# Kernel tuning notes

Hardware: AMD Instinct MI355X
Metric: run time of the kernel (lower is better)

Reference implementation:

```python
import jax, jax.numpy as jnp
import numpy as np
from jax import lax

KERNEL = 3
K = 3


def setup_inputs() -> dict:
    key = jax.random.key(0)
    xcorr = jax.random.normal(key, (16, 1, 256, 8192), dtype=jnp.float32)
    return {"xcorr": xcorr}


def reference(xcorr):
    # xcorr: [B, C, H, W] (W = lag axis)
    W = xcorr.shape[-1]
    nlag = W // 2
    # max_pool2d with kernel (1,KERNEL), stride 1, padding (0, KERNEL//2).
    # torch pads with -inf for max pooling.
    neg_inf = jnp.asarray(-jnp.inf, dtype=xcorr.dtype)
    pad = KERNEL // 2
    smax = lax.reduce_window(
        xcorr,
        neg_inf,
        lax.max,
        window_dimensions=(1, 1, 1, KERNEL),
        window_strides=(1, 1, 1, 1),
        padding=[(0, 0), (0, 0), (0, 0), (pad, pad)],
    )
    keep = (smax == xcorr).astype(xcorr.dtype)  # local-max NMS mask
    scores = xcorr * keep
    topk_scores, topk_inds = lax.top_k(scores, K)  # sorted descending, [B,C,H,K]
    top = topk_inds[..., 0]  # best peak index [B,C,H]
    nearby = jnp.clip(
        jnp.stack([top - 1, top, top + 1], axis=-1), 0, W - 1
    )  # [B,C,H,3]
    neighbor_score = jnp.take_along_axis(xcorr, nearby, axis=-1)
    topk_index = topk_inds - nlag
    return neighbor_score, topk_scores, topk_index
```

## Files before the change

### kernel.cpp

```cpp
#include <hip/hip_runtime.h>
#include <climits>
#include <cmath>


#define PW    8192
#define PNLAG (PW / 2)
#define BLOCK 256
#define QPT   (PW / 4 / BLOCK)

__device__ __forceinline__ bool better(float av, int ai, float bv, int bi) {
  return (av > bv) || ((av == bv) && (ai < bi));
}

__device__ __forceinline__ void insert3_full(float v, int i,
                                             float &v0, int &i0,
                                             float &v1, int &i1,
                                             float &v2, int &i2) {
  if (better(v, i, v2, i2)) {
    if (better(v, i, v1, i1)) {
      if (better(v, i, v0, i0)) {
        v2 = v1; i2 = i1; v1 = v0; i1 = i0; v0 = v; i0 = i;
      } else {
        v2 = v1; i2 = i1; v1 = v; i1 = i;
      }
    } else {
      v2 = v; i2 = i;
    }
  }
}

__device__ __forceinline__ void insert3_fast(float c, int ci,
                                             float &v0, int &i0,
                                             float &v1, int &i1,
                                             float &v2, int &i2) {
  const bool b2 = c > v2;
  const bool b1 = c > v1;
  const bool b0 = c > v0;
  v2 = b1 ? v1 : (b2 ? c : v2);  i2 = b1 ? i1 : (b2 ? ci : i2);
  v1 = b0 ? v0 : (b1 ? c : v1);  i1 = b0 ? i0 : (b1 ? ci : i1);
  v0 = b0 ? c  : v0;             i0 = b0 ? ci : i0;
}

__global__ __launch_bounds__(BLOCK)
void detect_peaks_kernel(const float* __restrict__ x,
                         float* __restrict__ out,
                         int rows) {
  __shared__ float rv[12];
  __shared__ int   ri[12];

  const int row = blockIdx.x;
  const int t   = threadIdx.x;
  const float* __restrict__ xr = x + (size_t)row * PW;
  const float4* __restrict__ xv = (const float4*)xr;

  float v0 = -INFINITY, v1 = -INFINITY, v2 = -INFINITY;
  int   i0 = INT_MAX,   i1 = INT_MAX,   i2 = INT_MAX;

#pragma unroll
  for (int j = 0; j < QPT; ++j) {
    const int q = j * BLOCK + t;
    const int p = q * 4;
    const float4 v = xv[q];
    const float left  = (p > 0)        ? xr[p - 1] : -INFINITY;
    const float right = (p + 4 < PW)   ? xr[p + 4] : -INFINITY;

    const float p01 = fmaxf(v.x, v.y);
    const float p12 = fmaxf(v.y, v.z);
    const float p23 = fmaxf(v.z, v.w);
    const float m0 = fmaxf(left, p01);
    const float m1 = fmaxf(p01, v.z);
    const float m2 = fmaxf(p12, v.w);
    const float m3 = fmaxf(p23, right);

    const float s0 = (v.x == m0) ? v.x : 0.0f;
    const float s1 = (v.y == m1) ? v.y : 0.0f;
    const float s2 = (v.z == m2) ? v.z : 0.0f;
    const float s3 = (v.w == m3) ? v.w : 0.0f;

    const bool  a01 = s0 >= s1;
    const float hiA = a01 ? s0 : s1;   const int hiAi = a01 ? p     : p + 1;
    const float loA = a01 ? s1 : s0;   const int loAi = a01 ? p + 1 : p;
    const bool  a23 = s2 >= s3;
    const float hiB = a23 ? s2 : s3;   const int hiBi = a23 ? p + 2 : p + 3;
    const float loB = a23 ? s3 : s2;   const int loBi = a23 ? p + 3 : p + 2;

    const bool  ab  = hiA >= hiB;
    const float c1  = ab ? hiA : hiB;  const int c1i = ab ? hiAi : hiBi;
    const bool  sb  = ab ? (loA >= hiB) : (hiA >= loB);
    const float c2  = ab ? (sb ? loA : hiB) : (sb ? hiA : loB);
    const int   c2i = ab ? (sb ? loAi : hiBi) : (sb ? hiAi : loBi);

    insert3_fast(c1, c1i, v0, i0, v1, i1, v2, i2);
    insert3_fast(c2, c2i, v0, i0, v1, i1, v2, i2);
  }

  const int lane = t & 63;
  const int wave = t >> 6;
#pragma unroll
  for (int off = 32; off > 0; off >>= 1) {
    float ov0 = __shfl_down(v0, off);
    int   oi0 = __shfl_down(i0, off);
    float ov1 = __shfl_down(v1, off);
    int   oi1 = __shfl_down(i1, off);
    float ov2 = __shfl_down(v2, off);
    int   oi2 = __shfl_down(i2, off);
    if (lane + off < 64) {
      insert3_full(ov0, oi0, v0, i0, v1, i1, v2, i2);
      insert3_full(ov1, oi1, v0, i0, v1, i1, v2, i2);
      insert3_full(ov2, oi2, v0, i0, v1, i1, v2, i2);
    }
  }

  if (lane == 0) {
    rv[wave * 3 + 0] = v0; ri[wave * 3 + 0] = i0;
    rv[wave * 3 + 1] = v1; ri[wave * 3 + 1] = i1;
    rv[wave * 3 + 2] = v2; ri[wave * 3 + 2] = i2;
  }
  __syncthreads();

  if (t == 0) {
#pragma unroll
    for (int w = 1; w < 4; ++w) {
      insert3_full(rv[w * 3 + 0], ri[w * 3 + 0], v0, i0, v1, i1, v2, i2);
      insert3_full(rv[w * 3 + 1], ri[w * 3 + 1], v0, i0, v1, i1, v2, i2);
      insert3_full(rv[w * 3 + 2], ri[w * 3 + 2], v0, i0, v1, i1, v2, i2);
    }

    float* __restrict__ nb = out;
    float* __restrict__ ts = out + (size_t)rows * 3;
    float* __restrict__ ti = out + (size_t)rows * 6;

    const int top = i0;
#pragma unroll
    for (int k = 0; k < 3; ++k) {
      int idx = top - 1 + k;
      idx = idx < 0 ? 0 : (idx > PW - 1 ? PW - 1 : idx);
      nb[row * 3 + k] = xr[idx];
    }
    ts[row * 3 + 0] = v0;
    ts[row * 3 + 1] = v1;
    ts[row * 3 + 2] = v2;
    ti[row * 3 + 0] = (float)(i0 - PNLAG);
    ti[row * 3 + 1] = (float)(i1 - PNLAG);
    ti[row * 3 + 2] = (float)(i2 - PNLAG);
  }
}

extern "C" void kernel_launch(void* const* d_in, const int* in_sizes, int n_in,
                              void* d_out, int out_size, void* d_ws, size_t ws_size,
                              hipStream_t stream) {
  const float* x = (const float*)d_in[0];
  float* out = (float*)d_out;
  const int rows = in_sizes[0] / PW;
  detect_peaks_kernel<<<rows, BLOCK, 0, stream>>>(x, out, rows);
}
```

Measured before the change: 247.4 us.

## Load wave-contiguous float4 chunks up front and get neighbors via lane shuffles

Each wave now owns a contiguous 512-float4 segment and issues all eight vector loads before computing. The per-element left/right neighbor values are obtained by cross-lane shuffles instead of separate scalar global loads, with only the wave-boundary elements loaded from memory. This removes redundant scalar loads and increases memory-level parallelism, at the cost of extra shuffle instructions and more registers held live.

```diff
diff --git a/kernel.cpp b/kernel.cpp
--- a/kernel.cpp
+++ b/kernel.cpp
@@ -6,7 +6,8 @@
 #define PW    8192
 #define PNLAG (PW / 2)
 #define BLOCK 256
-#define QPT   (PW / 4 / BLOCK)
+#define NW    4
+#define J     8
 
 __device__ __forceinline__ bool better(float av, int ai, float bv, int bi) {
   return (av > bv) || ((av == bv) && (ai < bi));
@@ -48,21 +49,39 @@
   __shared__ float rv[12];
   __shared__ int   ri[12];
 
-  const int row = blockIdx.x;
-  const int t   = threadIdx.x;
+  const int row  = blockIdx.x;
+  const int t    = threadIdx.x;
+  const int lane = t & 63;
+  const int wave = t >> 6;
   const float* __restrict__ xr = x + (size_t)row * PW;
   const float4* __restrict__ xv = (const float4*)xr;
+
+  const int waveQ = wave * (J * 64);
+
+  float4 q[J];
+#pragma unroll
+  for (int j = 0; j < J; ++j) {
+    q[j] = xv[waveQ + j * 64 + lane];
+  }
+  float leftEdge  = -INFINITY;
+  float rightEdge = -INFINITY;
+  if (lane == 0 && wave > 0)      leftEdge  = xr[waveQ * 4 - 1];
+  if (lane == 63 && wave < NW - 1) rightEdge = xr[(waveQ + J * 64) * 4];
 
   float v0 = -INFINITY, v1 = -INFINITY, v2 = -INFINITY;
   int   i0 = INT_MAX,   i1 = INT_MAX,   i2 = INT_MAX;
 
 #pragma unroll
-  for (int j = 0; j < QPT; ++j) {
-    const int q = j * BLOCK + t;
-    const int p = q * 4;
-    const float4 v = xv[q];
-    const float left  = (p > 0)        ? xr[p - 1] : -INFINITY;
-    const float right = (p + 4 < PW)   ? xr[p + 4] : -INFINITY;
+  for (int j = 0; j < J; ++j) {
+    const int p = (waveQ + j * 64 + lane) * 4;
+    const float4 v = q[j];
+
+    const float lu = __shfl_up(v.w, 1);
+    const float l0 = (j > 0) ? __shfl(q[j - 1].w, 63) : leftEdge;
+    const float left = (lane == 0) ? l0 : lu;
+    const float rd = __shfl_down(v.x, 1);
+    const float r0 = (j < J - 1) ? __shfl(q[j + 1].x, 0) : rightEdge;
+    const float right = (lane == 63) ? r0 : rd;
 
     const float p01 = fmaxf(v.x, v.y);
     const float p12 = fmaxf(v.y, v.z);
@@ -94,8 +113,6 @@
     insert3_fast(c2, c2i, v0, i0, v1, i1, v2, i2);
   }
 
-  const int lane = t & 63;
-  const int wave = t >> 6;
 #pragma unroll
   for (int off = 32; off > 0; off >>= 1) {
     float ov0 = __shfl_down(v0, off);
@@ -120,7 +137,7 @@
 
   if (t == 0) {
 #pragma unroll
-    for (int w = 1; w < 4; ++w) {
+    for (int w = 1; w < NW; ++w) {
       insert3_full(rv[w * 3 + 0], ri[w * 3 + 0], v0, i0, v1, i1, v2, i2);
       insert3_full(rv[w * 3 + 1], ri[w * 3 + 1], v0, i0, v1, i1, v2, i2);
       insert3_full(rv[w * 3 + 2], ri[w * 3 + 2], v0, i0, v1, i1, v2, i2);
```

New measurement: 239.8 us. 1.03x faster.

## Use persistent 1024-thread blocks with next-row prefetch and shuffle-based halos

Applied to the files above, without the earlier changes.

The kernel changes from one 256-thread block per row to a persistent grid of 512 blocks with 1024 threads each that loop over rows. Each block loads the next row's data while it processes the current one. Neighbour halo values now come from wave shuffles instead of redundant global loads, and the final reduction across waves runs in parallel in wave 0 rather than serially in thread 0. The aim is to hide memory latency and cut extra loads, at the cost of double-buffered shared memory, one barrier per row, and fewer distinct blocks in flight.

```diff
diff --git a/kernel.cpp b/kernel.cpp
--- a/kernel.cpp
+++ b/kernel.cpp
@@ -3,10 +3,11 @@
 #include <cmath>
 
 
-#define PW    8192
-#define PNLAG (PW / 2)
-#define BLOCK 256
-#define QPT   (PW / 4 / BLOCK)
+#define PW     8192
+#define PNLAG  (PW / 2)
+#define TPB    1024
+#define NWAVES 16
+#define GRID   512
 
 __device__ __forceinline__ bool better(float av, int ai, float bv, int bi) {
   return (av > bv) || ((av == bv) && (ai < bi));
@@ -41,108 +42,152 @@
   v0 = b0 ? c  : v0;             i0 = b0 ? ci : i0;
 }
 
-__global__ __launch_bounds__(BLOCK)
+__device__ __forceinline__ void quad_cands(const float4 v, float left, float right, int p,
+                                           float &v0, int &i0, float &v1, int &i1,
+                                           float &v2, int &i2) {
+  const float p01 = fmaxf(v.x, v.y);
+  const float p12 = fmaxf(v.y, v.z);
+  const float p23 = fmaxf(v.z, v.w);
+  const float m0 = fmaxf(left, p01);
+  const float m1 = fmaxf(p01, v.z);
+  const float m2 = fmaxf(p12, v.w);
+  const float m3 = fmaxf(p23, right);
+  const float s0 = (v.x == m0) ? v.x : 0.0f;
+  const float s1 = (v.y == m1) ? v.y : 0.0f;
+  const float s2 = (v.z == m2) ? v.z : 0.0f;
+  const float s3 = (v.w == m3) ? v.w : 0.0f;
+  const bool  a01 = s0 >= s1;
+  const float hiA = a01 ? s0 : s1;   const int hiAi = a01 ? p     : p + 1;
+  const float loA = a01 ? s1 : s0;   const int loAi = a01 ? p + 1 : p;
+  const bool  a23 = s2 >= s3;
+  const float hiB = a23 ? s2 : s3;   const int hiBi = a23 ? p + 2 : p + 3;
+  const float loB = a23 ? s3 : s2;   const int loBi = a23 ? p + 3 : p + 2;
+  const bool  ab  = hiA >= hiB;
+  const float c1  = ab ? hiA : hiB;  const int c1i = ab ? hiAi : hiBi;
+  const bool  sb  = ab ? (loA >= hiB) : (hiA >= loB);
+  const float c2  = ab ? (sb ? loA : hiB) : (sb ? hiA : loB);
+  const int   c2i = ab ? (sb ? loAi : hiBi) : (sb ? hiAi : loBi);
+  insert3_fast(c1, c1i, v0, i0, v1, i1, v2, i2);
+  insert3_fast(c2, c2i, v0, i0, v1, i1, v2, i2);
+}
+
+__global__ __launch_bounds__(TPB)
 void detect_peaks_kernel(const float* __restrict__ x,
                          float* __restrict__ out,
                          int rows) {
-  __shared__ float rv[12];
-  __shared__ int   ri[12];
-
-  const int row = blockIdx.x;
-  const int t   = threadIdx.x;
-  const float* __restrict__ xr = x + (size_t)row * PW;
-  const float4* __restrict__ xv = (const float4*)xr;
-
-  float v0 = -INFINITY, v1 = -INFINITY, v2 = -INFINITY;
-  int   i0 = INT_MAX,   i1 = INT_MAX,   i2 = INT_MAX;
+  __shared__ float sv[2][NWAVES][3];
+  __shared__ int   si[2][NWAVES][3];
+
+  const int t     = threadIdx.x;
+  const int lane  = t & 63;
+  const int wave  = t >> 6;
+  const int qAidx = wave * 128 + lane;
+  const int qBidx = qAidx + 64;
+  const int spanL = wave * 512;
+
+  float* __restrict__ nb = out;
+  float* __restrict__ ts = out + (size_t)rows * 3;
+  float* __restrict__ ti = out + (size_t)rows * 6;
+
+  int row = blockIdx.x;
+
+  const float* xr0 = x + (size_t)row * PW;
+  float4 qA = ((const float4*)xr0)[qAidx];
+  float4 qB = ((const float4*)xr0)[qBidx];
+  float  eL = (lane == 0  && wave > 0)          ? xr0[spanL - 1]   : -INFINITY;
+  float  eR = (lane == 63 && wave < NWAVES - 1) ? xr0[spanL + 512] : -INFINITY;
+
+  int pb = 0;
+  while (row < rows) {
+    const float* __restrict__ xr_cur = x + (size_t)row * PW;
+    const int nrow = row + GRID;
+
+    float4 qA2 = {0, 0, 0, 0}, qB2 = {0, 0, 0, 0};
+    float  eL2 = -INFINITY, eR2 = -INFINITY;
+    if (nrow < rows) {
+      const float* __restrict__ xn = x + (size_t)nrow * PW;
+      qA2 = ((const float4*)xn)[qAidx];
+      qB2 = ((const float4*)xn)[qBidx];
+      if (lane == 0  && wave > 0)          eL2 = xn[spanL - 1];
+      if (lane == 63 && wave < NWAVES - 1) eR2 = xn[spanL + 512];
+    }
+
+    const float luA = __shfl_up(qA.w, 1);
+    const float rdA = __shfl_down(qA.x, 1);
+    const float bxB = __shfl(qB.x, 0);
+    const float luB = __shfl_up(qB.w, 1);
+    const float rdB = __shfl_down(qB.x, 1);
+    const float awB = __shfl(qA.w, 63);
+
+    const float lA = (lane == 0)  ? eL  : luA;
+    const float rA = (lane == 63) ? bxB : rdA;
+    const float lB = (lane == 0)  ? awB : luB;
+    const float rB = (lane == 63) ? eR  : rdB;
+
+    float v0 = -INFINITY, v1 = -INFINITY, v2 = -INFINITY;
+    int   i0 = INT_MAX,   i1 = INT_MAX,   i2 = INT_MAX;
+    quad_cands(qA, lA, rA, qAidx * 4, v0, i0, v1, i1, v2, i2);
+    quad_cands(qB, lB, rB, qBidx * 4, v0, i0, v1, i1, v2, i2);
 
 #pragma unroll
-  for (int j = 0; j < QPT; ++j) {
-    const int q = j * BLOCK + t;
-    const int p = q * 4;
-    const float4 v = xv[q];
-    const float left  = (p > 0)        ? xr[p - 1] : -INFINITY;
-    const float right = (p + 4 < PW)   ? xr[p + 4] : -INFINITY;
-
-    const float p01 = fmaxf(v.x, v.y);
-    const float p12 = fmaxf(v.y, v.z);
-    const float p23 = fmaxf(v.z, v.w);
-    const float m0 = fmaxf(left, p01);
-    const float m1 = fmaxf(p01, v.z);
-    const float m2 = fmaxf(p12, v.w);
-    const float m3 = fmaxf(p23, right);
-
-    const float s0 = (v.x == m0) ? v.x : 0.0f;
-    const float s1 = (v.y == m1) ? v.y : 0.0f;
-    const float s2 = (v.z == m2) ? v.z : 0.0f;
-    const float s3 = (v.w == m3) ? v.w : 0.0f;
-
-    const bool  a01 = s0 >= s1;
-    const float hiA = a01 ? s0 : s1;   const int hiAi = a01 ? p     : p + 1;
-    const float loA = a01 ? s1 : s0;   const int loAi = a01 ? p + 1 : p;
-    const bool  a23 = s2 >= s3;
-    const float hiB = a23 ? s2 : s3;   const int hiBi = a23 ? p + 2 : p + 3;
-    const float loB = a23 ? s3 : s2;   const int loBi = a23 ? p + 3 : p + 2;
-
-    const bool  ab  = hiA >= hiB;
-    const float c1  = ab ? hiA : hiB;  const int c1i = ab ? hiAi : hiBi;
-    const bool  sb  = ab ? (loA >= hiB) : (hiA >= loB);
-    const float c2  = ab ? (sb ? loA : hiB) : (sb ? hiA : loB);
-    const int   c2i = ab ? (sb ? loAi : hiBi) : (sb ? hiAi : loBi);
-
-    insert3_fast(c1, c1i, v0, i0, v1, i1, v2, i2);
-    insert3_fast(c2, c2i, v0, i0, v1, i1, v2, i2);
-  }
-
-  const int lane = t & 63;
-  const int wave = t >> 6;
+    for (int off = 32; off > 0; off >>= 1) {
+      float ov0 = __shfl_down(v0, off);
+      int   oi0 = __shfl_down(i0, off);
+      float ov1 = __shfl_down(v1, off);
+      int   oi1 = __shfl_down(i1, off);
+      float ov2 = __shfl_down(v2, off);
+      int   oi2 = __shfl_down(i2, off);
+      if (lane + off < 64) {
+        insert3_full(ov0, oi0, v0, i0, v1, i1, v2, i2);
+        insert3_full(ov1, oi1, v0, i0, v1, i1, v2, i2);
+        insert3_full(ov2, oi2, v0, i0, v1, i1, v2, i2);
+      }
+    }
+    if (lane == 0) {
+      sv[pb][wave][0] = v0; si[pb][wave][0] = i0;
+      sv[pb][wave][1] = v1; si[pb][wave][1] = i1;
+      sv[pb][wave][2] = v2; si[pb][wave][2] = i2;
+    }
+    __syncthreads();
+
+    if (wave == 0) {
+      float mv = -INFINITY; int mi = INT_MAX;
+      if (lane < NWAVES * 3) {
+        mv = sv[pb][lane / 3][lane % 3];
+        mi = si[pb][lane / 3][lane % 3];
+      }
+      float w0 = mv,       w1 = -INFINITY, w2 = -INFINITY;
+      int   j0 = mi,       j1 = INT_MAX,   j2 = INT_MAX;
 #pragma unroll
-  for (int off = 32; off > 0; off >>= 1) {
-    float ov0 = __shfl_down(v0, off);
-    int   oi0 = __shfl_down(i0, off);
-    float ov1 = __shfl_down(v1, off);
-    int   oi1 = __shfl_down(i1, off);
-    float ov2 = __shfl_down(v2, off);
-    int   oi2 = __shfl_down(i2, off);
-    if (lane + off < 64) {
-      insert3_full(ov0, oi0, v0, i0, v1, i1, v2, i2);
-      insert3_full(ov1, oi1, v0, i0, v1, i1, v2, i2);
-      insert3_full(ov2, oi2, v0, i0, v1, i1, v2, i2);
-    }
-  }
-
-  if (lane == 0) {
-    rv[wave * 3 + 0] = v0; ri[wave * 3 + 0] = i0;
-    rv[wave * 3 + 1] = v1; ri[wave * 3 + 1] = i1;
-    rv[wave * 3 + 2] = v2; ri[wave * 3 + 2] = i2;
-  }
-  __syncthreads();
-
-  if (t == 0) {
-#pragma unroll
-    for (int w = 1; w < 4; ++w) {
-      insert3_full(rv[w * 3 + 0], ri[w * 3 + 0], v0, i0, v1, i1, v2, i2);
-      insert3_full(rv[w * 3 + 1], ri[w * 3 + 1], v0, i0, v1, i1, v2, i2);
-      insert3_full(rv[w * 3 + 2], ri[w * 3 + 2], v0, i0, v1, i1, v2, i2);
-    }
-
-    float* __restrict__ nb = out;
-    float* __restrict__ ts = out + (size_t)rows * 3;
-    float* __restrict__ ti = out + (size_t)rows * 6;
-
-    const int top = i0;
-#pragma unroll
-    for (int k = 0; k < 3; ++k) {
-      int idx = top - 1 + k;
-      idx = idx < 0 ? 0 : (idx > PW - 1 ? PW - 1 : idx);
-      nb[row * 3 + k] = xr[idx];
-    }
-    ts[row * 3 + 0] = v0;
-    ts[row * 3 + 1] = v1;
-    ts[row * 3 + 2] = v2;
-    ti[row * 3 + 0] = (float)(i0 - PNLAG);
-    ti[row * 3 + 1] = (float)(i1 - PNLAG);
-    ti[row * 3 + 2] = (float)(i2 - PNLAG);
+      for (int off = 32; off > 0; off >>= 1) {
+        float o0 = __shfl_down(w0, off);
+        int   k0 = __shfl_down(j0, off);
+        float o1 = __shfl_down(w1, off);
+        int   k1 = __shfl_down(j1, off);
+        float o2 = __shfl_down(w2, off);
+        int   k2 = __shfl_down(j2, off);
+        if (lane + off < 64) {
+          insert3_full(o0, k0, w0, j0, w1, j1, w2, j2);
+          insert3_full(o1, k1, w0, j0, w1, j1, w2, j2);
+          insert3_full(o2, k2, w0, j0, w1, j1, w2, j2);
+        }
+      }
+      const float b0 = __shfl(w0, 0);  const int c0 = __shfl(j0, 0);
+      const float b1 = __shfl(w1, 0);  const int c1 = __shfl(j1, 0);
+      const float b2 = __shfl(w2, 0);  const int c2 = __shfl(j2, 0);
+      if (lane < 3) {
+        int idx = c0 - 1 + lane;
+        idx = idx < 0 ? 0 : (idx > PW - 1 ? PW - 1 : idx);
+        nb[row * 3 + lane] = xr_cur[idx];
+        ts[row * 3 + lane] = (lane == 0) ? b0 : (lane == 1) ? b1 : b2;
+        const int tix      = (lane == 0) ? c0 : (lane == 1) ? c1 : c2;
+        ti[row * 3 + lane] = (float)(tix - PNLAG);
+      }
+    }
+
+    qA = qA2; qB = qB2; eL = eL2; eR = eR2;
+    row = nrow;
+    pb ^= 1;
   }
 }
 
@@ -152,5 +197,5 @@
   const float* x = (const float*)d_in[0];
   float* out = (float*)d_out;
   const int rows = in_sizes[0] / PW;
-  detect_peaks_kernel<<<rows, BLOCK, 0, stream>>>(x, out, rows);
-}
+  detect_peaks_kernel<<<GRID, TPB, 0, stream>>>(x, out, rows);
+}
```

New measurement: 420.2 us. 1.7x slower.

## Split row top-k into per-wave scan kernel plus combine kernel

Applied to the files above, without the earlier changes.

Replaces the one-block-per-row kernel with two launches. The first assigns one wave per 256-element slice, gets neighbour values through lane shuffles instead of extra global loads, and writes each wave's top-3 candidates to workspace. The second merges the 32 per-wave candidate sets of each row with one wave per row. This is meant to expose more parallelism and cut redundant edge loads, at the cost of a second launch, a workspace round trip, and a hard-coded row count of 4096.

```diff
diff --git a/kernel.cpp b/kernel.cpp
--- a/kernel.cpp
+++ b/kernel.cpp
@@ -5,8 +5,10 @@
 
 #define PW    8192
 #define PNLAG (PW / 2)
-#define BLOCK 256
-#define QPT   (PW / 4 / BLOCK)
+#define ROWS  4096
+#define WPR   32
+#define GRID1 (ROWS * WPR / 4)
+#define GRID2 (ROWS / 4)
 
 __device__ __forceinline__ bool better(float av, int ai, float bv, int bi) {
   return (av > bv) || ((av == bv) && (ai < bi));
@@ -29,73 +31,8 @@
   }
 }
 
-__device__ __forceinline__ void insert3_fast(float c, int ci,
-                                             float &v0, int &i0,
-                                             float &v1, int &i1,
-                                             float &v2, int &i2) {
-  const bool b2 = c > v2;
-  const bool b1 = c > v1;
-  const bool b0 = c > v0;
-  v2 = b1 ? v1 : (b2 ? c : v2);  i2 = b1 ? i1 : (b2 ? ci : i2);
-  v1 = b0 ? v0 : (b1 ? c : v1);  i1 = b0 ? i0 : (b1 ? ci : i1);
-  v0 = b0 ? c  : v0;             i0 = b0 ? ci : i0;
-}
-
-__global__ __launch_bounds__(BLOCK)
-void detect_peaks_kernel(const float* __restrict__ x,
-                         float* __restrict__ out,
-                         int rows) {
-  __shared__ float rv[12];
-  __shared__ int   ri[12];
-
-  const int row = blockIdx.x;
-  const int t   = threadIdx.x;
-  const float* __restrict__ xr = x + (size_t)row * PW;
-  const float4* __restrict__ xv = (const float4*)xr;
-
-  float v0 = -INFINITY, v1 = -INFINITY, v2 = -INFINITY;
-  int   i0 = INT_MAX,   i1 = INT_MAX,   i2 = INT_MAX;
-
-#pragma unroll
-  for (int j = 0; j < QPT; ++j) {
-    const int q = j * BLOCK + t;
-    const int p = q * 4;
-    const float4 v = xv[q];
-    const float left  = (p > 0)        ? xr[p - 1] : -INFINITY;
-    const float right = (p + 4 < PW)   ? xr[p + 4] : -INFINITY;
-
-    const float p01 = fmaxf(v.x, v.y);
-    const float p12 = fmaxf(v.y, v.z);
-    const float p23 = fmaxf(v.z, v.w);
-    const float m0 = fmaxf(left, p01);
-    const float m1 = fmaxf(p01, v.z);
-    const float m2 = fmaxf(p12, v.w);
-    const float m3 = fmaxf(p23, right);
-
-    const float s0 = (v.x == m0) ? v.x : 0.0f;
-    const float s1 = (v.y == m1) ? v.y : 0.0f;
-    const float s2 = (v.z == m2) ? v.z : 0.0f;
-    const float s3 = (v.w == m3) ? v.w : 0.0f;
-
-    const bool  a01 = s0 >= s1;
-    const float hiA = a01 ? s0 : s1;   const int hiAi = a01 ? p     : p + 1;
-    const float loA = a01 ? s1 : s0;   const int loAi = a01 ? p + 1 : p;
-    const bool  a23 = s2 >= s3;
-    const float hiB = a23 ? s2 : s3;   const int hiBi = a23 ? p + 2 : p + 3;
-    const float loB = a23 ? s3 : s2;   const int loBi = a23 ? p + 3 : p + 2;
-
-    const bool  ab  = hiA >= hiB;
-    const float c1  = ab ? hiA : hiB;  const int c1i = ab ? hiAi : hiBi;
-    const bool  sb  = ab ? (loA >= hiB) : (hiA >= loB);
-    const float c2  = ab ? (sb ? loA : hiB) : (sb ? hiA : loB);
-    const int   c2i = ab ? (sb ? loAi : hiBi) : (sb ? hiAi : loBi);
-
-    insert3_fast(c1, c1i, v0, i0, v1, i1, v2, i2);
-    insert3_fast(c2, c2i, v0, i0, v1, i1, v2, i2);
-  }
-
-  const int lane = t & 63;
-  const int wave = t >> 6;
+__device__ __forceinline__ void wave_merge3(float &v0, int &i0, float &v1, int &i1,
+                                            float &v2, int &i2, int lane) {
 #pragma unroll
   for (int off = 32; off > 0; off >>= 1) {
     float ov0 = __shfl_down(v0, off);
@@ -110,26 +47,92 @@
       insert3_full(ov2, oi2, v0, i0, v1, i1, v2, i2);
     }
   }
+}
+
+__global__ __launch_bounds__(256)
+void scan_kernel(const float* __restrict__ x, float2* __restrict__ pw) {
+  const int t    = threadIdx.x;
+  const int lane = t & 63;
+  const int wv   = t >> 6;
+  const int gw   = blockIdx.x * 4 + wv;
+  const int row  = gw >> 5;
+  const int wsl  = gw & 31;
+  const float* __restrict__ xr = x + (size_t)row * PW;
+
+  const int q = wsl * 64 + lane;
+  const int p = q * 4;
+  const float4 v = ((const float4*)xr)[q];
+
+  const float eL = (lane == 0  && wsl > 0)       ? xr[p - 1] : -INFINITY;
+  const float eR = (lane == 63 && wsl < WPR - 1) ? xr[p + 4] : -INFINITY;
+  const float lu = __shfl_up(v.w, 1);
+  const float rd = __shfl_down(v.x, 1);
+  const float left  = (lane == 0)  ? eL : lu;
+  const float right = (lane == 63) ? eR : rd;
+
+  const float p01 = fmaxf(v.x, v.y);
+  const float p12 = fmaxf(v.y, v.z);
+  const float p23 = fmaxf(v.z, v.w);
+  const float m0 = fmaxf(left, p01);
+  const float m1 = fmaxf(p01, v.z);
+  const float m2 = fmaxf(p12, v.w);
+  const float m3 = fmaxf(p23, right);
+
+  const float s0 = (v.x == m0) ? v.x : 0.0f;
+  const float s1 = (v.y == m1) ? v.y : 0.0f;
+  const float s2 = (v.z == m2) ? v.z : 0.0f;
+  const float s3 = (v.w == m3) ? v.w : 0.0f;
+
+  const bool  a01 = s0 >= s1;
+  const float hiA = a01 ? s0 : s1;   const int hiAi = a01 ? p     : p + 1;
+  const float loA = a01 ? s1 : s0;   const int loAi = a01 ? p + 1 : p;
+  const bool  a23 = s2 >= s3;
+  const float hiB = a23 ? s2 : s3;   const int hiBi = a23 ? p + 2 : p + 3;
+  const float loB = a23 ? s3 : s2;   const int loBi = a23 ? p + 3 : p + 2;
+
+  const bool  ab  = hiA >= hiB;
+  float v0 = ab ? hiA : hiB;         int i0 = ab ? hiAi : hiBi;
+  const bool  sb  = ab ? (loA >= hiB) : (hiA >= loB);
+  float v1 = ab ? (sb ? loA : hiB) : (sb ? hiA : loB);
+  int   i1 = ab ? (sb ? loAi : hiBi) : (sb ? hiAi : loBi);
+  float v2 = -INFINITY;              int i2 = INT_MAX;
+
+  wave_merge3(v0, i0, v1, i1, v2, i2, lane);
 
   if (lane == 0) {
-    rv[wave * 3 + 0] = v0; ri[wave * 3 + 0] = i0;
-    rv[wave * 3 + 1] = v1; ri[wave * 3 + 1] = i1;
-    rv[wave * 3 + 2] = v2; ri[wave * 3 + 2] = i2;
+    float2* c = pw + (size_t)gw * 3;
+    c[0] = make_float2(v0, __int_as_float(i0));
+    c[1] = make_float2(v1, __int_as_float(i1));
+    c[2] = make_float2(v2, __int_as_float(i2));
   }
-  __syncthreads();
+}
 
-  if (t == 0) {
-#pragma unroll
-    for (int w = 1; w < 4; ++w) {
-      insert3_full(rv[w * 3 + 0], ri[w * 3 + 0], v0, i0, v1, i1, v2, i2);
-      insert3_full(rv[w * 3 + 1], ri[w * 3 + 1], v0, i0, v1, i1, v2, i2);
-      insert3_full(rv[w * 3 + 2], ri[w * 3 + 2], v0, i0, v1, i1, v2, i2);
-    }
+__global__ __launch_bounds__(256)
+void combine_kernel(const float* __restrict__ x, const float2* __restrict__ pw,
+                    float* __restrict__ out) {
+  const int t    = threadIdx.x;
+  const int lane = t & 63;
+  const int wv   = t >> 6;
+  const int row  = blockIdx.x * 4 + wv;
+  const float* __restrict__ xr = x + (size_t)row * PW;
+  const float2* __restrict__ c = pw + (size_t)row * (WPR * 3);
 
+  float v0 = -INFINITY, v1 = -INFINITY, v2 = -INFINITY;
+  int   i0 = INT_MAX,   i1 = INT_MAX,   i2 = INT_MAX;
+
+  const float2 a = c[lane];
+  insert3_full(a.x, __float_as_int(a.y), v0, i0, v1, i1, v2, i2);
+  if (lane < WPR * 3 - 64) {
+    const float2 b = c[64 + lane];
+    insert3_full(b.x, __float_as_int(b.y), v0, i0, v1, i1, v2, i2);
+  }
+
+  wave_merge3(v0, i0, v1, i1, v2, i2, lane);
+
+  if (lane == 0) {
     float* __restrict__ nb = out;
-    float* __restrict__ ts = out + (size_t)rows * 3;
-    float* __restrict__ ti = out + (size_t)rows * 6;
-
+    float* __restrict__ ts = out + (size_t)ROWS * 3;
+    float* __restrict__ ti = out + (size_t)ROWS * 6;
     const int top = i0;
 #pragma unroll
     for (int k = 0; k < 3; ++k) {
@@ -151,6 +154,7 @@
                               hipStream_t stream) {
   const float* x = (const float*)d_in[0];
   float* out = (float*)d_out;
-  const int rows = in_sizes[0] / PW;
-  detect_peaks_kernel<<<rows, BLOCK, 0, stream>>>(x, out, rows);
+  float2* pw = (float2*)d_ws;
+  scan_kernel<<<GRID1, 256, 0, stream>>>(x, pw);
+  combine_kernel<<<GRID2, 256, 0, stream>>>(x, pw, out);
 }
```

After: 612.0 us. 2.47x slower.
